# Kernel optimization log

Hardware: AMD Instinct MI355X
Metric: run time of the kernel (lower is better)

## Reference

```python
import jax, jax.numpy as jnp
import numpy as np
from jax import lax


def setup_inputs() -> dict:
    key = jax.random.key(0)
    kx, kw = jax.random.split(key)
    x = jax.random.normal(kx, (32, 3, 8192), dtype=jnp.float32)
    weight = jax.random.normal(kw, (128, 3, 64), dtype=jnp.float32)
    return {"x": x, "weight": weight}


def reference(x, weight):
    # x: [B, C, L], weight: [O, C, K]
    K = weight.shape[2]
    # Cross-correlation (conv1d, no bias, valid padding): [B, O, L-K+1]
    conv_out = lax.conv_general_dilated(
        x, weight, window_strides=(1,), padding='VALID',
        dimension_numbers=('NCH', 'OIH', 'NCH'))
    # Half squared norm of each shapelet: [O]
    w_norm = jnp.sum(weight ** 2, axis=(1, 2)) / 2
    # Half squared norm of each length-K window, via cumulative sums
    # (avoids materializing the [B, C, W, K] unfold tensor)
    sq = jnp.sum(x ** 2, axis=1)               # [B, L]
    c = jnp.pad(jnp.cumsum(sq, axis=1), ((0, 0), (1, 0)))  # [B, L+1]
    win_norm = (c[:, K:] - c[:, :-K]) / 2      # [B, L-K+1]
    # features = conv_out - (||w||^2/2 + ||window||^2/2)
    features = conv_out - w_norm[None, :, None] - win_norm[:, None, :]
    # global max-pool over time, then *(-2) -> min squared distance
    return -2.0 * jnp.max(features, axis=-1)   # [B, O]
```

## Files before the change

kernel.cpp:

```cpp
#include <hip/hip_runtime.h>
#include <float.h>

#define BB 32
#define LL 8192
#define OO 128
#define KK 64
#define WW (LL - KK + 1)
#define NCH 3
#define GX 11

typedef __attribute__((ext_vector_type(8))) short short8;
typedef __attribute__((ext_vector_type(4))) float f32x4;

union AB { int4 i4; int i[4]; short8 v; };

static __device__ __forceinline__ unsigned int f2bf(float f) {
    unsigned int u = __builtin_bit_cast(unsigned int, f);
    return (u + 0x7FFFu + ((u >> 16) & 1u)) >> 16;
}

static __device__ __forceinline__ void stage_load(const float* __restrict__ x, int b, int T0,
                                                  int tid, float4* v) {
    v[0] = make_float4(0.f, 0.f, 0.f, 0.f);
    v[1] = v[0];
    v[2] = v[0];
    if (tid < 80) {
        int l = T0 + 4 * tid;
        if (l < LL) {
            const float* p = x + (size_t)b * 3 * LL + l;
            v[0] = *(const float4*)(p);
            v[1] = *(const float4*)(p + LL);
            v[2] = *(const float4*)(p + 2 * LL);
        }
    }
}

static __device__ __forceinline__ void stage_store(int tid, const float4* v,
                                                   unsigned short* xl, float* sql, float* Pl) {
    if (tid >= 80) return;
    #pragma unroll
    for (int c = 0; c < 3; ++c) {
        uint2 pk;
        pk.x = f2bf(v[c].x) | (f2bf(v[c].y) << 16);
        pk.y = f2bf(v[c].z) | (f2bf(v[c].w) << 16);
        *(uint2*)(xl + c * 320 + tid * 4) = pk;
    }
    float4 sq4;
    sq4.x = fmaf(v[2].x, v[2].x, fmaf(v[1].x, v[1].x, v[0].x * v[0].x));
    sq4.y = fmaf(v[2].y, v[2].y, fmaf(v[1].y, v[1].y, v[0].y * v[0].y));
    sq4.z = fmaf(v[2].z, v[2].z, fmaf(v[1].z, v[1].z, v[0].z * v[0].z));
    sq4.w = fmaf(v[2].w, v[2].w, fmaf(v[1].w, v[1].w, v[0].w * v[0].w));
    *(float4*)(sql + tid * 4) = sq4;
    float s4 = (sq4.x + sq4.y) + (sq4.z + sq4.w);
    float s8 = s4 + __shfl_xor(s4, 1, 64);
    if ((tid & 1) == 0) Pl[tid >> 1] = s8;
}

__global__ __launch_bounds__(256, 3) void shapeconv_main(const float* __restrict__ x,
                                                         const float* __restrict__ w,
                                                         float* __restrict__ partial) {
    __shared__ __align__(16) unsigned short w_lds[64 * 192];
    __shared__ __align__(16) unsigned short x_lds[2][3 * 320];
    __shared__ __align__(16) float sq_lds[2][320];
    __shared__ __align__(16) float P_lds[2][40];
    __shared__ float wnp[4][64];
    __shared__ float mred[64];

    const int tcx = blockIdx.x;
    const int ob = blockIdx.y;
    const int b  = blockIdx.z;
    const int tid = threadIdx.x;
    const int wv = tid >> 6;
    const int lane = tid & 63;
    const int wo = wv & 1, wt = wv >> 1;
    const int n  = lane & 15;
    const int qp = lane >> 4;
    const int Tb = tcx * (NCH * 256);

    float4 sv[3];
    stage_load(x, b, Tb, tid, sv);

    {
        const int o2 = tid & 63;
        const int row = tid >> 6;
        const float* wb = w + ((size_t)(ob * 64 + o2)) * 192;
        float wsq = 0.f;
        #pragma unroll
        for (int i = 0; i < 6; ++i) {
            int g = tid + 256 * i;
            int ksqp = g >> 6;
            int ks = ksqp >> 2, qq = ksqp & 3;
            int c = ks >> 1, h = ks & 1;
            const float4* p = (const float4*)(wb + c * 64 + h * 32 + qq * 8);
            float4 v0 = p[0], v1 = p[1];
            int4 pk;
            pk.x = (int)(f2bf(v0.x) | (f2bf(v0.y) << 16));
            pk.y = (int)(f2bf(v0.z) | (f2bf(v0.w) << 16));
            pk.z = (int)(f2bf(v1.x) | (f2bf(v1.y) << 16));
            pk.w = (int)(f2bf(v1.z) | (f2bf(v1.w) << 16));
            ((int4*)w_lds)[g] = pk;
            wsq = fmaf(v0.x, v0.x, wsq); wsq = fmaf(v0.y, v0.y, wsq);
            wsq = fmaf(v0.z, v0.z, wsq); wsq = fmaf(v0.w, v0.w, wsq);
            wsq = fmaf(v1.x, v1.x, wsq); wsq = fmaf(v1.y, v1.y, wsq);
            wsq = fmaf(v1.z, v1.z, wsq); wsq = fmaf(v1.w, v1.w, wsq);
        }
        wnp[row][o2] = wsq;
    }

    stage_store(tid, sv, x_lds[0], sq_lds[0], P_lds[0]);
    __syncthreads();

    float nw[2][4];
    #pragma unroll
    for (int ot = 0; ot < 2; ++ot)
        #pragma unroll
        for (int rg = 0; rg < 4; ++rg) {
            int o = 32 * wo + 16 * ot + 4 * qp + rg;
            nw[ot][rg] = 0.5f * ((wnp[0][o] + wnp[1][o]) + (wnp[2][o] + wnp[3][o]));
        }

    float m2[2][4];
    #pragma unroll
    for (int ot = 0; ot < 2; ++ot)
        #pragma unroll
        for (int rg = 0; rg < 4; ++rg) m2[ot][rg] = -FLT_MAX;

    for (int ci = 0; ci < NCH; ++ci) {
        const int bsel = ci & 1;
        const int T0 = Tb + ci * 256;
        const bool more = (ci + 1 < NCH);
        if (more) stage_load(x, b, T0 + 256, tid, sv);

        float wl[8];
        {
            const float* sqp = sq_lds[bsel];
            const float* Pl  = P_lds[bsel];
            const int mi = 16 * wt + n;
            float S = 0.f;
            #pragma unroll
            for (int i = 0; i < 8; ++i) S += Pl[mi + i];
            #pragma unroll
            for (int r = 0; r < 8; ++r) {
                wl[r] = (T0 + 8 * mi + r < WW) ? 0.5f * S : 1e30f;
                if (r < 7) S += sqp[8 * mi + 64 + r] - sqp[8 * mi + r];
            }
        }

        f32x4 acc[2][8];
        #pragma unroll
        for (int ot = 0; ot < 2; ++ot)
            #pragma unroll
            for (int rg = 0; rg < 4; ++rg)
                #pragma unroll
                for (int r = 0; r < 8; ++r)
                    acc[ot][r][rg] = -nw[ot][rg] - wl[r];

        const char* xb = (const char*)x_lds[bsel];
        __builtin_amdgcn_s_setprio(1);
        #pragma unroll
        for (int ks = 0; ks < 6; ++ks) {
            int c = ks >> 1, h = ks & 1;
            int e0b = c * 640 + 256 * wt + 64 * h + 16 * (n + qp);
            int4 Ea = *(const int4*)(xb + e0b);
            int4 Eb = *(const int4*)(xb + e0b + 16);
            int D[8] = {Ea.x, Ea.y, Ea.z, Ea.w, Eb.x, Eb.y, Eb.z, Eb.w};
            AB a0, a1;
            const int4* wq = (const int4*)w_lds + (ks * 4 + qp) * 64 + 32 * wo;
            a0.i4 = wq[n];
            a1.i4 = wq[16 + n];
            #pragma unroll
            for (int r = 0; r < 8; ++r) {
                AB bf;
                int s = r >> 1;
                if ((r & 1) == 0) {
                    bf.i[0] = D[s]; bf.i[1] = D[s + 1]; bf.i[2] = D[s + 2]; bf.i[3] = D[s + 3];
                } else {
                    #pragma unroll
                    for (int d = 0; d < 4; ++d)
                        bf.i[d] = (int)(((unsigned)D[s + d] >> 16) | ((unsigned)D[s + d + 1] << 16));
                }
                acc[0][r] = __builtin_amdgcn_mfma_f32_16x16x32_bf16(a0.v, bf.v, acc[0][r], 0, 0, 0);
                acc[1][r] = __builtin_amdgcn_mfma_f32_16x16x32_bf16(a1.v, bf.v, acc[1][r], 0, 0, 0);
            }
        }
        __builtin_amdgcn_s_setprio(0);

        #pragma unroll
        for (int ot = 0; ot < 2; ++ot)
            #pragma unroll
            for (int rg = 0; rg < 4; ++rg) {
                float mm = m2[ot][rg];
                #pragma unroll
                for (int r = 0; r < 8; ++r) mm = fmaxf(mm, acc[ot][r][rg]);
                m2[ot][rg] = mm;
            }

        if (more) {
            stage_store(tid, sv, x_lds[1 - bsel], sq_lds[1 - bsel], P_lds[1 - bsel]);
            __syncthreads();
        }
    }

    #pragma unroll
    for (int s = 1; s <= 8; s <<= 1)
        #pragma unroll
        for (int ot = 0; ot < 2; ++ot)
            #pragma unroll
            for (int rg = 0; rg < 4; ++rg)
                m2[ot][rg] = fmaxf(m2[ot][rg], __shfl_xor(m2[ot][rg], s, 64));

    if (wt == 1 && n == 0) {
        #pragma unroll
        for (int ot = 0; ot < 2; ++ot)
            #pragma unroll
            for (int rg = 0; rg < 4; ++rg)
                mred[32 * wo + 16 * ot + 4 * qp + rg] = m2[ot][rg];
    }
    __syncthreads();
    if (wt == 0 && n == 0) {
        #pragma unroll
        for (int ot = 0; ot < 2; ++ot)
            #pragma unroll
            for (int rg = 0; rg < 4; ++rg) {
                int oi = 32 * wo + 16 * ot + 4 * qp + rg;
                float v = fmaxf(m2[ot][rg], mred[oi]);
                partial[((size_t)(b * GX + tcx) * 2 + ob) * 64 + oi] = v;
            }
    }
}

__global__ __launch_bounds__(256) void reduce_kernel(const float* __restrict__ partial,
                                                     float* __restrict__ out) {
    int idx = blockIdx.x * 256 + threadIdx.x;
    int b = idx >> 7, o = idx & 127;
    const float* pp = partial + ((size_t)b * GX * 2 + (o >> 6)) * 64 + (o & 63);
    float mx = -FLT_MAX;
    #pragma unroll
    for (int t = 0; t < GX; ++t) mx = fmaxf(mx, pp[(size_t)t * 128]);
    out[idx] = -2.f * mx;
}

extern "C" void kernel_launch(void* const* d_in, const int* in_sizes, int n_in,
                              void* d_out, int out_size, void* d_ws, size_t ws_size,
                              hipStream_t stream) {
    const float* x = (const float*)d_in[0];
    const float* w = (const float*)d_in[1];
    float* out = (float*)d_out;

    float* partial = (float*)d_ws;

    dim3 grid(GX, 2, BB);
    shapeconv_main<<<grid, 256, 0, stream>>>(x, w, partial);
    reduce_kernel<<<16, 256, 0, stream>>>(partial, out);
}
```

Before: 72.92 us.

## Give each wave private x staging buffers to drop per-chunk block barriers

Each wave now loads, converts and stores its own 192-element slice of x (with halo) into per-wave LDS buffers, so the main loop no longer needs __syncthreads between chunks. The window-norm computation moves after the MFMAs and the weight-norm subtraction is deferred to the final write, so accumulators start at zero. The loop also skips chunks that lie entirely beyond the valid output range, and bf16 packing uses the HIP intrinsic. The cost is redundant global loads and conversions for the overlapping halo between the two waves sharing a time range, plus more LDS.

New measurement: 99.10 us. +35.9%, slower.

```diff
diff --git a/kernel.cpp b/kernel.cpp
--- a/kernel.cpp
+++ b/kernel.cpp
@@ -1,4 +1,5 @@
 #include <hip/hip_runtime.h>
+#include <hip/hip_bf16.h>
 #include <float.h>
 
 #define BB 32
@@ -14,55 +15,74 @@
 
 union AB { int4 i4; int i[4]; short8 v; };
 
-static __device__ __forceinline__ unsigned int f2bf(float f) {
-    unsigned int u = __builtin_bit_cast(unsigned int, f);
-    return (u + 0x7FFFu + ((u >> 16) & 1u)) >> 16;
-}
-
-static __device__ __forceinline__ void stage_load(const float* __restrict__ x, int b, int T0,
-                                                  int tid, float4* v) {
-    v[0] = make_float4(0.f, 0.f, 0.f, 0.f);
-    v[1] = v[0];
-    v[2] = v[0];
-    if (tid < 80) {
-        int l = T0 + 4 * tid;
-        if (l < LL) {
-            const float* p = x + (size_t)b * 3 * LL + l;
-            v[0] = *(const float4*)(p);
-            v[1] = *(const float4*)(p + LL);
-            v[2] = *(const float4*)(p + 2 * LL);
-        }
-    }
-}
-
-static __device__ __forceinline__ void stage_store(int tid, const float4* v,
-                                                   unsigned short* xl, float* sql, float* Pl) {
-    if (tid >= 80) return;
+static __device__ __forceinline__ unsigned int pkbf(float a, float b) {
+    union { __hip_bfloat162 h; unsigned int u; } cv;
+    cv.h = __float22bfloat162_rn(make_float2(a, b));
+    return cv.u;
+}
+
+struct Stage { float2 va[3]; float2 vb[3]; };
+
+static __device__ __forceinline__ void stage_load(const float* __restrict__ x, int b, int T0w,
+                                                  int lane, Stage& st) {
     #pragma unroll
     for (int c = 0; c < 3; ++c) {
-        uint2 pk;
-        pk.x = f2bf(v[c].x) | (f2bf(v[c].y) << 16);
-        pk.y = f2bf(v[c].z) | (f2bf(v[c].w) << 16);
-        *(uint2*)(xl + c * 320 + tid * 4) = pk;
-    }
-    float4 sq4;
-    sq4.x = fmaf(v[2].x, v[2].x, fmaf(v[1].x, v[1].x, v[0].x * v[0].x));
-    sq4.y = fmaf(v[2].y, v[2].y, fmaf(v[1].y, v[1].y, v[0].y * v[0].y));
-    sq4.z = fmaf(v[2].z, v[2].z, fmaf(v[1].z, v[1].z, v[0].z * v[0].z));
-    sq4.w = fmaf(v[2].w, v[2].w, fmaf(v[1].w, v[1].w, v[0].w * v[0].w));
-    *(float4*)(sql + tid * 4) = sq4;
-    float s4 = (sq4.x + sq4.y) + (sq4.z + sq4.w);
-    float s8 = s4 + __shfl_xor(s4, 1, 64);
-    if ((tid & 1) == 0) Pl[tid >> 1] = s8;
+        st.va[c] = make_float2(0.f, 0.f);
+        st.vb[c] = make_float2(0.f, 0.f);
+    }
+    const float* xb = x + (size_t)b * 3 * LL;
+    int e0 = T0w + 2 * lane;
+    if (e0 < LL) {
+        #pragma unroll
+        for (int c = 0; c < 3; ++c) st.va[c] = *(const float2*)(xb + c * LL + e0);
+    }
+    int e1 = T0w + 128 + 2 * lane;
+    if (lane < 32 && e1 < LL) {
+        #pragma unroll
+        for (int c = 0; c < 3; ++c) st.vb[c] = *(const float2*)(xb + c * LL + e1);
+    }
+}
+
+static __device__ __forceinline__ void stage_store(int lane, const Stage& st,
+                                                   unsigned short* xw, float* sqw, float* Pw) {
+    float sx = 0.f, sy = 0.f;
+    #pragma unroll
+    for (int c = 0; c < 3; ++c) {
+        *(unsigned int*)(xw + c * 192 + 2 * lane) = pkbf(st.va[c].x, st.va[c].y);
+        sx = fmaf(st.va[c].x, st.va[c].x, sx);
+        sy = fmaf(st.va[c].y, st.va[c].y, sy);
+    }
+    *(float2*)(sqw + 2 * lane) = make_float2(sx, sy);
+    float p2 = sx + sy;
+    p2 += __shfl_xor(p2, 1, 64);
+    p2 += __shfl_xor(p2, 2, 64);
+    if ((lane & 3) == 0) Pw[lane >> 2] = p2;
+    float tx = 0.f, ty = 0.f;
+    unsigned int pk[3];
+    #pragma unroll
+    for (int c = 0; c < 3; ++c) {
+        tx = fmaf(st.vb[c].x, st.vb[c].x, tx);
+        ty = fmaf(st.vb[c].y, st.vb[c].y, ty);
+        pk[c] = pkbf(st.vb[c].x, st.vb[c].y);
+    }
+    if (lane < 32) {
+        #pragma unroll
+        for (int c = 0; c < 3; ++c) *(unsigned int*)(xw + c * 192 + 128 + 2 * lane) = pk[c];
+        *(float2*)(sqw + 128 + 2 * lane) = make_float2(tx, ty);
+    }
+    float q2 = tx + ty;
+    q2 += __shfl_xor(q2, 1, 64);
+    q2 += __shfl_xor(q2, 2, 64);
+    if (lane < 32 && (lane & 3) == 0) Pw[16 + (lane >> 2)] = q2;
 }
 
 __global__ __launch_bounds__(256, 3) void shapeconv_main(const float* __restrict__ x,
                                                          const float* __restrict__ w,
                                                          float* __restrict__ partial) {
     __shared__ __align__(16) unsigned short w_lds[64 * 192];
-    __shared__ __align__(16) unsigned short x_lds[2][3 * 320];
-    __shared__ __align__(16) float sq_lds[2][320];
-    __shared__ __align__(16) float P_lds[2][40];
+    __shared__ __align__(16) unsigned short xw_lds[4][2][3 * 192];
+    __shared__ __align__(16) float sq_lds[4][2][192];
+    __shared__ __align__(16) float P_lds[4][2][24];
     __shared__ float wnp[4][64];
     __shared__ float mred[64];
 
@@ -76,9 +96,10 @@
     const int n  = lane & 15;
     const int qp = lane >> 4;
     const int Tb = tcx * (NCH * 256);
-
-    float4 sv[3];
-    stage_load(x, b, Tb, tid, sv);
+    const int nch_eff = (WW - Tb + 255) >> 8 < NCH ? (WW - Tb + 255) >> 8 : NCH;
+
+    Stage st;
+    stage_load(x, b, Tb + 128 * wt, lane, st);
 
     {
         const int o2 = tid & 63;
@@ -94,10 +115,10 @@
             const float4* p = (const float4*)(wb + c * 64 + h * 32 + qq * 8);
             float4 v0 = p[0], v1 = p[1];
             int4 pk;
-            pk.x = (int)(f2bf(v0.x) | (f2bf(v0.y) << 16));
-            pk.y = (int)(f2bf(v0.z) | (f2bf(v0.w) << 16));
-            pk.z = (int)(f2bf(v1.x) | (f2bf(v1.y) << 16));
-            pk.w = (int)(f2bf(v1.z) | (f2bf(v1.w) << 16));
+            pk.x = (int)pkbf(v0.x, v0.y);
+            pk.y = (int)pkbf(v0.z, v0.w);
+            pk.z = (int)pkbf(v1.x, v1.y);
+            pk.w = (int)pkbf(v1.z, v1.w);
             ((int4*)w_lds)[g] = pk;
             wsq = fmaf(v0.x, v0.x, wsq); wsq = fmaf(v0.y, v0.y, wsq);
             wsq = fmaf(v0.z, v0.z, wsq); wsq = fmaf(v0.w, v0.w, wsq);
@@ -107,7 +128,7 @@
         wnp[row][o2] = wsq;
     }
 
-    stage_store(tid, sv, x_lds[0], sq_lds[0], P_lds[0]);
+    stage_store(lane, st, xw_lds[wv][0], sq_lds[wv][0], P_lds[wv][0]);
     __syncthreads();
 
     float nw[2][4];
@@ -125,42 +146,25 @@
         #pragma unroll
         for (int rg = 0; rg < 4; ++rg) m2[ot][rg] = -FLT_MAX;
 
-    for (int ci = 0; ci < NCH; ++ci) {
-        const int bsel = ci & 1;
-        const int T0 = Tb + ci * 256;
-        const bool more = (ci + 1 < NCH);
-        if (more) stage_load(x, b, T0 + 256, tid, sv);
-
-        float wl[8];
-        {
-            const float* sqp = sq_lds[bsel];
-            const float* Pl  = P_lds[bsel];
-            const int mi = 16 * wt + n;
-            float S = 0.f;
-            #pragma unroll
-            for (int i = 0; i < 8; ++i) S += Pl[mi + i];
-            #pragma unroll
-            for (int r = 0; r < 8; ++r) {
-                wl[r] = (T0 + 8 * mi + r < WW) ? 0.5f * S : 1e30f;
-                if (r < 7) S += sqp[8 * mi + 64 + r] - sqp[8 * mi + r];
-            }
-        }
+    for (int ci = 0; ci < nch_eff; ++ci) {
+        const int bs = ci & 1;
+        const int T0w = Tb + ci * 256 + 128 * wt;
+        const bool more = (ci + 1 < nch_eff);
+        if (more) stage_load(x, b, T0w + 256, lane, st);
 
         f32x4 acc[2][8];
         #pragma unroll
         for (int ot = 0; ot < 2; ++ot)
             #pragma unroll
-            for (int rg = 0; rg < 4; ++rg)
-                #pragma unroll
-                for (int r = 0; r < 8; ++r)
-                    acc[ot][r][rg] = -nw[ot][rg] - wl[r];
-
-        const char* xb = (const char*)x_lds[bsel];
+            for (int r = 0; r < 8; ++r)
+                acc[ot][r] = (f32x4){0.f, 0.f, 0.f, 0.f};
+
+        const char* xb = (const char*)xw_lds[wv][bs];
         __builtin_amdgcn_s_setprio(1);
         #pragma unroll
         for (int ks = 0; ks < 6; ++ks) {
             int c = ks >> 1, h = ks & 1;
-            int e0b = c * 640 + 256 * wt + 64 * h + 16 * (n + qp);
+            int e0b = c * 384 + 64 * h + 16 * (n + qp);
             int4 Ea = *(const int4*)(xb + e0b);
             int4 Eb = *(const int4*)(xb + e0b + 16);
             int D[8] = {Ea.x, Ea.y, Ea.z, Ea.w, Eb.x, Eb.y, Eb.z, Eb.w};
@@ -185,20 +189,32 @@
         }
         __builtin_amdgcn_s_setprio(0);
 
+        float wl[8];
+        {
+            const float* sqp = sq_lds[wv][bs];
+            const float* Pl  = P_lds[wv][bs];
+            float S = 0.f;
+            #pragma unroll
+            for (int i = 0; i < 8; ++i) S += Pl[n + i];
+            #pragma unroll
+            for (int r = 0; r < 8; ++r) {
+                wl[r] = (T0w + 8 * n + r < WW) ? 0.5f * S : 1e30f;
+                if (r < 7) S += sqp[8 * n + 64 + r] - sqp[8 * n + r];
+            }
+        }
+
         #pragma unroll
         for (int ot = 0; ot < 2; ++ot)
             #pragma unroll
             for (int rg = 0; rg < 4; ++rg) {
                 float mm = m2[ot][rg];
                 #pragma unroll
-                for (int r = 0; r < 8; ++r) mm = fmaxf(mm, acc[ot][r][rg]);
+                for (int r = 0; r < 8; ++r) mm = fmaxf(mm, acc[ot][r][rg] - wl[r]);
                 m2[ot][rg] = mm;
             }
 
-        if (more) {
-            stage_store(tid, sv, x_lds[1 - bsel], sq_lds[1 - bsel], P_lds[1 - bsel]);
-            __syncthreads();
-        }
+        if (more)
+            stage_store(lane, st, xw_lds[wv][1 - bs], sq_lds[wv][1 - bs], P_lds[wv][1 - bs]);
     }
 
     #pragma unroll
@@ -223,7 +239,7 @@
             #pragma unroll
             for (int rg = 0; rg < 4; ++rg) {
                 int oi = 32 * wo + 16 * ot + 4 * qp + rg;
-                float v = fmaxf(m2[ot][rg], mred[oi]);
+                float v = fmaxf(m2[ot][rg], mred[oi]) - nw[ot][rg];
                 partial[((size_t)(b * GX + tcx) * 2 + ob) * 64 + oi] = v;
             }
     }
```
